# Performance work log

Hardware: AMD Instinct MI355X
Metric: run time of the kernel (lower is better)

The kernel has to match this reference:

```python
import jax, jax.numpy as jnp
import numpy as np

BN_EPS = 1e-5


def setup_inputs() -> dict:
    key = jax.random.key(0)
    ks = jax.random.split(key, 12)
    B, C, S, M = 128, 512, 128, 512  # batch, model_dim, spatial_size, middle_ss
    lim_in = 1.0 / np.sqrt(S)   # torch Linear init bound, fan_in = S
    lim_mid = 1.0 / np.sqrt(M)
    return {
        "query": jax.random.normal(ks[0], (B, C, S), jnp.float32),
        "key":   jax.random.normal(ks[1], (B, C, S), jnp.float32),
        "value": jax.random.normal(ks[2], (B, C, S), jnp.float32),
        "Wq": jax.random.uniform(ks[3], (M, S), jnp.float32, -lim_in, lim_in),
        "bq": jax.random.uniform(ks[4], (M,), jnp.float32, -lim_in, lim_in),
        "Wk": jax.random.uniform(ks[5], (M, S), jnp.float32, -lim_in, lim_in),
        "bk": jax.random.uniform(ks[6], (M,), jnp.float32, -lim_in, lim_in),
        "Wv": jax.random.uniform(ks[7], (M, S), jnp.float32, -lim_in, lim_in),
        "bv": jax.random.uniform(ks[8], (M,), jnp.float32, -lim_in, lim_in),
        "Wf": jax.random.uniform(ks[9], (S, M), jnp.float32, -lim_mid, lim_mid),
        "bf": jax.random.uniform(ks[10], (S,), jnp.float32, -lim_mid, lim_mid),
        "gamma": jnp.ones((C,), jnp.float32),
        "beta": jnp.zeros((C,), jnp.float32),
    }


def reference(query, key, value, Wq, bq, Wk, bk, Wv, bv, Wf, bf, gamma, beta):
    residual = value                                  # [B, C, S]
    q = jnp.einsum('bcs,ms->bcm', query, Wq) + bq     # [B, C, M]
    k = jnp.einsum('bcs,ms->bcm', key, Wk) + bk
    v = jnp.einsum('bcs,ms->bcm', value, Wv) + bv
    scale = k.shape[-1] ** (-0.5)
    scores = jnp.einsum('bim,bjm->bij', q, k) * scale  # [B, C, C]
    attention = jax.nn.softmax(scores, axis=2)
    context = jnp.einsum('bij,bjm->bim', attention, v)  # [B, C, M]
    out = jnp.einsum('bcm,sm->bcs', context, Wf) + bf    # [B, C, S]
    # BatchNorm1d (training mode): stats over (batch, spatial) per channel
    mean = jnp.mean(out, axis=(0, 2), keepdims=True)
    var = jnp.mean(jnp.square(out - mean), axis=(0, 2), keepdims=True)
    out = (out - mean) * jax.lax.rsqrt(var + BN_EPS)
    out = out * gamma[None, :, None] + beta[None, :, None]
    out = jax.nn.relu(out)
    out = residual + out
    return (out, attention)
```

## Files before the change

### kernel.cpp

```cpp
#include <hip/hip_runtime.h>
#include <math.h>

#define B_  128
#define C_  512
#define S_  128
#define M_  512
#define BN_EPS 1e-5f

typedef __attribute__((ext_vector_type(8))) short   short8;
typedef __attribute__((ext_vector_type(4))) float   floatx4;
typedef __attribute__((ext_vector_type(4))) unsigned short ushort4v;

__device__ __forceinline__ unsigned short f2bu(float f) {
    union { float f; unsigned int u; } c; c.f = f;
    unsigned int u = c.u;
    return (unsigned short)((u + 0x7fffu + ((u >> 16) & 1u)) >> 16);
}

__global__ __launch_bounds__(256)
void f2bf_kernel(const float* __restrict__ in, unsigned short* __restrict__ out, long n8)
{
    const long i = (long)blockIdx.x * 256 + threadIdx.x;
    if (i >= n8) return;
    const float4* p = (const float4*)in + 2 * i;
    const float4 x = p[0], y = p[1];
    ushort4v u0, u1;
    u0.x = f2bu(x.x); u0.y = f2bu(x.y); u0.z = f2bu(x.z); u0.w = f2bu(x.w);
    u1.x = f2bu(y.x); u1.y = f2bu(y.y); u1.z = f2bu(y.z); u1.w = f2bu(y.w);
    ((ushort4v*)out)[2 * i]     = u0;
    ((ushort4v*)out)[2 * i + 1] = u1;
}

__global__ __launch_bounds__(256)
void gemm_bf16(const unsigned short* __restrict__ A, const unsigned short* __restrict__ Bm,
               const float* __restrict__ bias, void* __restrict__ Cc,
               int M, int N, int K, int ldA, int ldB, int ldC,
               long sA, long sB, long sC, float scale, int outMode)
{
    const int bz = blockIdx.z;
    A  += (long)bz * sA;
    Bm += (long)bz * sB;

    __shared__ unsigned short As[128][72];
    __shared__ unsigned short Bs[128][72];

    const int t    = threadIdx.x;
    const int lane = t & 63;
    const int wave = t >> 6;
    const int wm   = (wave >> 1) * 64;
    const int wn   = (wave & 1) * 64;
    const int lrow = lane & 15;
    const int quad = lane >> 4;
    const int row0 = blockIdx.x * 128;
    const int col0 = blockIdx.y * 128;

    floatx4 acc[4][4] = {};

    const int srow = t >> 3;
    const int skc  = (t & 7) * 8;

    for (int k0 = 0; k0 < K; k0 += 64) {
        #pragma unroll
        for (int i = 0; i < 4; ++i) {
            const int r = srow + i * 32;
            *(short8*)&As[r][skc] =
                *(const short8*)(A + (long)(row0 + r) * ldA + k0 + skc);
            *(short8*)&Bs[r][skc] =
                *(const short8*)(Bm + (long)(col0 + r) * ldB + k0 + skc);
        }
        __syncthreads();

        #pragma unroll
        for (int kb = 0; kb < 2; ++kb) {
            short8 af[4], bfr[4];
            #pragma unroll
            for (int i = 0; i < 4; ++i)
                af[i]  = *(const short8*)&As[wm + i * 16 + lrow][kb * 32 + quad * 8];
            #pragma unroll
            for (int j = 0; j < 4; ++j)
                bfr[j] = *(const short8*)&Bs[wn + j * 16 + lrow][kb * 32 + quad * 8];
            #pragma unroll
            for (int i = 0; i < 4; ++i)
                #pragma unroll
                for (int j = 0; j < 4; ++j)
                    acc[i][j] = __builtin_amdgcn_mfma_f32_16x16x32_bf16(
                        af[i], bfr[j], acc[i][j], 0, 0, 0);
        }
        __syncthreads();
    }

    #pragma unroll
    for (int j = 0; j < 4; ++j) {
        const int col = col0 + wn + j * 16 + lrow;
        const float bv = bias ? bias[col] : 0.0f;
        #pragma unroll
        for (int i = 0; i < 4; ++i) {
            const int rbase = row0 + wm + i * 16 + quad * 4;
            #pragma unroll
            for (int reg = 0; reg < 4; ++reg) {
                const float val = acc[i][j][reg] * scale + bv;
                const int r = rbase + reg;
                if (outMode == 0) {
                    ((float*)Cc)[(long)bz * sC + (long)r * ldC + col] = val;
                } else if (outMode == 1) {
                    ((unsigned short*)Cc)[(long)bz * sC + (long)r * ldC + col] = f2bu(val);
                } else {
                    ((unsigned short*)Cc)[((long)(r >> 9)) * 65536 + (long)col * 512 + (r & 511)] = f2bu(val);
                }
            }
        }
    }
}

__global__ __launch_bounds__(256)
void softmax_kernel(float* __restrict__ attn, unsigned short* __restrict__ attn_bf)
{
    const int row  = blockIdx.x * 4 + (threadIdx.x >> 6);
    const int lane = threadIdx.x & 63;
    float4* p = (float4*)(attn + (long)row * 512);

    float4 a = p[lane];
    float4 b = p[lane + 64];

    float mx = fmaxf(fmaxf(fmaxf(a.x, a.y), fmaxf(a.z, a.w)),
                     fmaxf(fmaxf(b.x, b.y), fmaxf(b.z, b.w)));
    #pragma unroll
    for (int off = 1; off < 64; off <<= 1)
        mx = fmaxf(mx, __shfl_xor(mx, off));

    a.x = expf(a.x - mx); a.y = expf(a.y - mx);
    a.z = expf(a.z - mx); a.w = expf(a.w - mx);
    b.x = expf(b.x - mx); b.y = expf(b.y - mx);
    b.z = expf(b.z - mx); b.w = expf(b.w - mx);

    float sum = a.x + a.y + a.z + a.w + b.x + b.y + b.z + b.w;
    #pragma unroll
    for (int off = 1; off < 64; off <<= 1)
        sum += __shfl_xor(sum, off);

    const float inv = 1.0f / sum;
    a.x *= inv; a.y *= inv; a.z *= inv; a.w *= inv;
    b.x *= inv; b.y *= inv; b.z *= inv; b.w *= inv;

    p[lane]      = a;
    p[lane + 64] = b;

    ushort4v u0, u1;
    u0.x = f2bu(a.x); u0.y = f2bu(a.y); u0.z = f2bu(a.z); u0.w = f2bu(a.w);
    u1.x = f2bu(b.x); u1.y = f2bu(b.y); u1.z = f2bu(b.z); u1.w = f2bu(b.w);
    ushort4v* q = (ushort4v*)(attn_bf + (long)row * 512);
    q[lane]      = u0;
    q[lane + 64] = u1;
}

__global__ __launch_bounds__(256)
void bn_stats_kernel(const float* __restrict__ outp, float* __restrict__ stats)
{
    const int c   = blockIdx.x;
    const int tid = threadIdx.x;
    float s = 0.f, ss = 0.f;
    for (int idx = tid; idx < B_ * S_; idx += 256) {
        const int b  = idx >> 7;
        const int sp = idx & 127;
        const float x = outp[((long)b * C_ + c) * S_ + sp];
        s  += x;
        ss += x * x;
    }
    __shared__ float shs[256];
    __shared__ float shss[256];
    shs[tid] = s; shss[tid] = ss;
    __syncthreads();
    for (int off = 128; off > 0; off >>= 1) {
        if (tid < off) { shs[tid] += shs[tid + off]; shss[tid] += shss[tid + off]; }
        __syncthreads();
    }
    if (tid == 0) {
        const float n    = (float)(B_ * S_);
        const float mean = shs[0] / n;
        const float var  = shss[0] / n - mean * mean;
        stats[c]      = mean;
        stats[C_ + c] = rsqrtf(var + BN_EPS);
    }
}

__global__ __launch_bounds__(256)
void bn_apply_kernel(const float* __restrict__ outp, const float* __restrict__ value,
                     const float* __restrict__ stats, const float* __restrict__ gamma,
                     const float* __restrict__ beta, float* __restrict__ out)
{
    const long i4 = (long)blockIdx.x * 256 + threadIdx.x;
    const int  c  = (int)((i4 >> 5) & (C_ - 1));

    const float mean = stats[c];
    const float istd = stats[C_ + c];
    const float g    = gamma[c] * istd;
    const float bc   = beta[c] - mean * g;

    const float4 x = ((const float4*)outp)[i4];
    const float4 r = ((const float4*)value)[i4];
    float4 y;
    y.x = fmaxf(fmaf(x.x, g, bc), 0.f) + r.x;
    y.y = fmaxf(fmaf(x.y, g, bc), 0.f) + r.y;
    y.z = fmaxf(fmaf(x.z, g, bc), 0.f) + r.z;
    y.w = fmaxf(fmaf(x.w, g, bc), 0.f) + r.w;
    ((float4*)out)[i4] = y;
}

extern "C" void kernel_launch(void* const* d_in, const int* in_sizes, int n_in,
                              void* d_out, int out_size, void* d_ws, size_t ws_size,
                              hipStream_t stream)
{
    const float* query = (const float*)d_in[0];
    const float* key   = (const float*)d_in[1];
    const float* value = (const float*)d_in[2];
    const float* Wq    = (const float*)d_in[3];
    const float* bq    = (const float*)d_in[4];
    const float* Wk    = (const float*)d_in[5];
    const float* bk    = (const float*)d_in[6];
    const float* Wv    = (const float*)d_in[7];
    const float* bv    = (const float*)d_in[8];
    const float* Wf    = (const float*)d_in[9];
    const float* bf    = (const float*)d_in[10];
    const float* gamma = (const float*)d_in[11];
    const float* beta  = (const float*)d_in[12];

    const long BC  = (long)B_ * C_;
    const long BCM = BC * M_;
    const long BCS = BC * S_;
    const long BCC = BC * C_;

    unsigned short* w      = (unsigned short*)d_ws;
    unsigned short* q_bf   = w;
    unsigned short* k_bf   = q_bf + BCM;
    unsigned short* v2_bf  = k_bf + BCM;
    unsigned short* attnbf = v2_bf + BCM;
    unsigned short* vwT    = attnbf + BCC;
    unsigned short* qin    = vwT + (long)B_ * S_ * C_;
    unsigned short* kin    = qin + BCS;
    unsigned short* vin    = kin + BCS;
    unsigned short* Wq_bf  = vin + BCS;
    unsigned short* Wk_bf  = Wq_bf + (long)M_ * S_;
    unsigned short* Wv_bf  = Wk_bf + (long)M_ * S_;
    unsigned short* Wf_bf  = Wv_bf + (long)M_ * S_;
    float* outp  = (float*)(Wf_bf + (long)S_ * M_);
    float* stats = outp + BCS;

    float* out0 = (float*)d_out;
    float* attn = out0 + BCS;

    const float scale = 1.0f / sqrtf((float)M_);
    dim3 blk(256);

    f2bf_kernel<<<dim3(BCS / 8 / 256), blk, 0, stream>>>(query, qin, BCS / 8);
    f2bf_kernel<<<dim3(BCS / 8 / 256), blk, 0, stream>>>(key,   kin, BCS / 8);
    f2bf_kernel<<<dim3(BCS / 8 / 256), blk, 0, stream>>>(value, vin, BCS / 8);
    f2bf_kernel<<<dim3(32), blk, 0, stream>>>(Wq, Wq_bf, (long)M_ * S_ / 8);
    f2bf_kernel<<<dim3(32), blk, 0, stream>>>(Wk, Wk_bf, (long)M_ * S_ / 8);
    f2bf_kernel<<<dim3(32), blk, 0, stream>>>(Wv, Wv_bf, (long)M_ * S_ / 8);
    f2bf_kernel<<<dim3(32), blk, 0, stream>>>(Wf, Wf_bf, (long)S_ * M_ / 8);

    gemm_bf16<<<dim3(512, 4, 1), blk, 0, stream>>>(
        qin, Wq_bf, bq, q_bf,  (int)BC, M_, S_, S_, S_, M_, 0, 0, 0, 1.0f, 1);
    gemm_bf16<<<dim3(512, 4, 1), blk, 0, stream>>>(
        kin, Wk_bf, bk, k_bf,  (int)BC, M_, S_, S_, S_, M_, 0, 0, 0, 1.0f, 1);
    gemm_bf16<<<dim3(512, 4, 1), blk, 0, stream>>>(
        vin, Wv_bf, bv, v2_bf, (int)BC, M_, S_, S_, S_, M_, 0, 0, 0, 1.0f, 1);

    gemm_bf16<<<dim3(4, 4, 128), blk, 0, stream>>>(
        q_bf, k_bf, nullptr, attn, C_, C_, M_, M_, M_, C_,
        (long)C_ * M_, (long)C_ * M_, (long)C_ * C_, scale, 0);

    softmax_kernel<<<dim3(BC / 4), blk, 0, stream>>>(attn, attnbf);

    gemm_bf16<<<dim3(512, 1, 1), blk, 0, stream>>>(
        v2_bf, Wf_bf, bf, vwT, (int)BC, S_, M_, M_, M_, 0, 0, 0, 0, 1.0f, 2);

    gemm_bf16<<<dim3(4, 1, 128), blk, 0, stream>>>(
        attnbf, vwT, nullptr, outp, C_, S_, C_, C_, C_, S_,
        (long)C_ * C_, (long)S_ * C_, (long)C_ * S_, 1.0f, 0);

    bn_stats_kernel<<<dim3(C_), blk, 0, stream>>>(outp, stats);

    bn_apply_kernel<<<dim3(BCS / 4 / 256), blk, 0, stream>>>(
        outp, value, stats, gamma, beta, out0);
}
```

Baseline: 649.0 us.

## Fuse scores GEMM with softmax, use direct-to-LDS loads with swizzle, batch conversions

Replaces the separate scores GEMM and softmax kernels with one 1024-thread kernel. It computes a 128x512 score tile per block and does the row max and sum through shared-memory reductions, so the fp32 scores are no longer written and then read back. The generic GEMM now loads straight into LDS via global_load_lds with an XOR-swizzled layout instead of padding, and carries occupancy hints. The Wf projection is recast so vwT comes out in a plain row-major layout without the scattered transposed stores. The seven fp32-to-bf16 conversion launches are merged into two, trading fewer launches for more complex kernels and higher register/LDS pressure.

```diff
diff --git a/kernel.cpp b/kernel.cpp
--- a/kernel.cpp
+++ b/kernel.cpp
@@ -17,11 +17,25 @@
     return (unsigned short)((u + 0x7fffu + ((u >> 16) & 1u)) >> 16);
 }
 
+__device__ __forceinline__ void gload_lds16(const unsigned short* g, unsigned short* l)
+{
+    __builtin_amdgcn_global_load_lds(
+        (const __attribute__((address_space(1))) unsigned int*)g,
+        (__attribute__((address_space(3))) unsigned int*)l,
+        16, 0, 0);
+}
+
 __global__ __launch_bounds__(256)
-void f2bf_kernel(const float* __restrict__ in, unsigned short* __restrict__ out, long n8)
+void f2bf3_kernel(const float* __restrict__ q, const float* __restrict__ k,
+                  const float* __restrict__ v,
+                  unsigned short* __restrict__ qo, unsigned short* __restrict__ ko,
+                  unsigned short* __restrict__ vo)
 {
     const long i = (long)blockIdx.x * 256 + threadIdx.x;
-    if (i >= n8) return;
+    const float* in; unsigned short* out;
+    if (blockIdx.y == 0)      { in = q; out = qo; }
+    else if (blockIdx.y == 1) { in = k; out = ko; }
+    else                      { in = v; out = vo; }
     const float4* p = (const float4*)in + 2 * i;
     const float4 x = p[0], y = p[1];
     ushort4v u0, u1;
@@ -32,17 +46,40 @@
 }
 
 __global__ __launch_bounds__(256)
-void gemm_bf16(const unsigned short* __restrict__ A, const unsigned short* __restrict__ Bm,
+void f2bfw_kernel(const float* __restrict__ w0, const float* __restrict__ w1,
+                  const float* __restrict__ w2, const float* __restrict__ w3,
+                  unsigned short* __restrict__ o0, unsigned short* __restrict__ o1,
+                  unsigned short* __restrict__ o2, unsigned short* __restrict__ o3)
+{
+    const long i = (long)blockIdx.x * 256 + threadIdx.x;
+    const float* in; unsigned short* out;
+    if (blockIdx.y == 0)      { in = w0; out = o0; }
+    else if (blockIdx.y == 1) { in = w1; out = o1; }
+    else if (blockIdx.y == 2) { in = w2; out = o2; }
+    else                      { in = w3; out = o3; }
+    const float4* p = (const float4*)in + 2 * i;
+    const float4 x = p[0], y = p[1];
+    ushort4v u0, u1;
+    u0.x = f2bu(x.x); u0.y = f2bu(x.y); u0.z = f2bu(x.z); u0.w = f2bu(x.w);
+    u1.x = f2bu(y.x); u1.y = f2bu(y.y); u1.z = f2bu(y.z); u1.w = f2bu(y.w);
+    ((ushort4v*)out)[2 * i]     = u0;
+    ((ushort4v*)out)[2 * i + 1] = u1;
+}
+
+__global__ __launch_bounds__(256, 4)
+void gemm_bf16(const unsigned short* __restrict__ A,
+               const unsigned short* __restrict__ Bm,
                const float* __restrict__ bias, void* __restrict__ Cc,
-               int M, int N, int K, int ldA, int ldB, int ldC,
-               long sA, long sB, long sC, float scale, int outMode)
+               int K, int ldA, int ldB, int ldC,
+               long sA, long sB, long sC, float scale,
+               int outMode, int biasRow)
 {
     const int bz = blockIdx.z;
     A  += (long)bz * sA;
     Bm += (long)bz * sB;
 
-    __shared__ unsigned short As[128][72];
-    __shared__ unsigned short Bs[128][72];
+    __shared__ __attribute__((aligned(16))) unsigned short As[128 * 64];
+    __shared__ __attribute__((aligned(16))) unsigned short Bs[128 * 64];
 
     const int t    = threadIdx.x;
     const int lane = t & 63;
@@ -54,37 +91,41 @@
     const int row0 = blockIdx.x * 128;
     const int col0 = blockIdx.y * 128;
 
+    const int slr = lane >> 3;
+    const int scg = (lane & 7) ^ slr;
+
     floatx4 acc[4][4] = {};
 
-    const int srow = t >> 3;
-    const int skc  = (t & 7) * 8;
-
     for (int k0 = 0; k0 < K; k0 += 64) {
         #pragma unroll
         for (int i = 0; i < 4; ++i) {
-            const int r = srow + i * 32;
-            *(short8*)&As[r][skc] =
-                *(const short8*)(A + (long)(row0 + r) * ldA + k0 + skc);
-            *(short8*)&Bs[r][skc] =
-                *(const short8*)(Bm + (long)(col0 + r) * ldB + k0 + skc);
+            const int r = wave * 32 + i * 8 + slr;
+            gload_lds16(A  + (long)(row0 + r) * ldA + k0 + scg * 8,
+                        As + (wave * 256 + i * 64) * 8);
+            gload_lds16(Bm + (long)(col0 + r) * ldB + k0 + scg * 8,
+                        Bs + (wave * 256 + i * 64) * 8);
         }
         __syncthreads();
 
         #pragma unroll
         for (int kb = 0; kb < 2; ++kb) {
-            short8 af[4], bfr[4];
-            #pragma unroll
-            for (int i = 0; i < 4; ++i)
-                af[i]  = *(const short8*)&As[wm + i * 16 + lrow][kb * 32 + quad * 8];
-            #pragma unroll
-            for (int j = 0; j < 4; ++j)
-                bfr[j] = *(const short8*)&Bs[wn + j * 16 + lrow][kb * 32 + quad * 8];
-            #pragma unroll
-            for (int i = 0; i < 4; ++i)
+            short8 af[4];
+            #pragma unroll
+            for (int i = 0; i < 4; ++i) {
+                const int r  = wm + i * 16 + lrow;
+                const int pg = r * 8 + ((kb * 4 + quad) ^ (r & 7));
+                af[i] = *(const short8*)(As + pg * 8);
+            }
+            #pragma unroll
+            for (int j = 0; j < 4; ++j) {
+                const int r  = wn + j * 16 + lrow;
+                const int pg = r * 8 + ((kb * 4 + quad) ^ (r & 7));
+                const short8 bf8 = *(const short8*)(Bs + pg * 8);
                 #pragma unroll
-                for (int j = 0; j < 4; ++j)
+                for (int i = 0; i < 4; ++i)
                     acc[i][j] = __builtin_amdgcn_mfma_f32_16x16x32_bf16(
-                        af[i], bfr[j], acc[i][j], 0, 0, 0);
+                        af[i], bf8, acc[i][j], 0, 0, 0);
+            }
         }
         __syncthreads();
     }
@@ -92,65 +133,153 @@
     #pragma unroll
     for (int j = 0; j < 4; ++j) {
         const int col = col0 + wn + j * 16 + lrow;
-        const float bv = bias ? bias[col] : 0.0f;
         #pragma unroll
         for (int i = 0; i < 4; ++i) {
             const int rbase = row0 + wm + i * 16 + quad * 4;
             #pragma unroll
             for (int reg = 0; reg < 4; ++reg) {
-                const float val = acc[i][j][reg] * scale + bv;
                 const int r = rbase + reg;
-                if (outMode == 0) {
-                    ((float*)Cc)[(long)bz * sC + (long)r * ldC + col] = val;
-                } else if (outMode == 1) {
-                    ((unsigned short*)Cc)[(long)bz * sC + (long)r * ldC + col] = f2bu(val);
-                } else {
-                    ((unsigned short*)Cc)[((long)(r >> 9)) * 65536 + (long)col * 512 + (r & 511)] = f2bu(val);
-                }
+                float v = acc[i][j][reg] * scale;
+                if (bias) v += biasRow ? bias[r] : bias[col];
+                if (outMode == 0)
+                    ((float*)Cc)[(long)bz * sC + (long)r * ldC + col] = v;
+                else
+                    ((unsigned short*)Cc)[(long)bz * sC + (long)r * ldC + col] = f2bu(v);
             }
         }
     }
 }
 
-__global__ __launch_bounds__(256)
-void softmax_kernel(float* __restrict__ attn, unsigned short* __restrict__ attn_bf)
-{
-    const int row  = blockIdx.x * 4 + (threadIdx.x >> 6);
-    const int lane = threadIdx.x & 63;
-    float4* p = (float4*)(attn + (long)row * 512);
-
-    float4 a = p[lane];
-    float4 b = p[lane + 64];
-
-    float mx = fmaxf(fmaxf(fmaxf(a.x, a.y), fmaxf(a.z, a.w)),
-                     fmaxf(fmaxf(b.x, b.y), fmaxf(b.z, b.w)));
+__global__ __launch_bounds__(1024, 4)
+void scores_softmax(const unsigned short* __restrict__ Q,
+                    const unsigned short* __restrict__ Kb,
+                    float* __restrict__ attn, unsigned short* __restrict__ attnbf,
+                    float scale)
+{
+    const int b    = blockIdx.y;
+    const int row0 = blockIdx.x * 128;
+    Q      += ((long)b * C_ + row0) * M_;
+    Kb     += (long)b * C_ * M_;
+    attn   += (long)b * C_ * C_;
+    attnbf += (long)b * C_ * C_;
+
+    __shared__ __attribute__((aligned(16))) unsigned short Qs[128 * 32];
+    __shared__ __attribute__((aligned(16))) unsigned short Ks[512 * 32];
+    __shared__ float red[128][8];
+
+    const int t    = threadIdx.x;
+    const int lane = t & 63;
+    const int wave = t >> 6;
+    const int wr   = wave >> 3;
+    const int wc   = wave & 7;
+    const int lrow = lane & 15;
+    const int quad = lane >> 4;
+
+    const int slr = lane >> 2;
+    const int scg = (lane & 3) ^ (slr & 3);
+
+    floatx4 acc[4][4] = {};
+
+    for (int k0 = 0; k0 < M_; k0 += 32) {
+        #pragma unroll
+        for (int ii = 0; ii < 2; ++ii) {
+            const int idx = wave * 2 + ii;
+            const int r   = idx * 16 + slr;
+            gload_lds16(Kb + (long)r * M_ + k0 + scg * 8,
+                        Ks + idx * 512);
+        }
+        if (wave < 8) {
+            const int r = wave * 16 + slr;
+            gload_lds16(Q + (long)r * M_ + k0 + scg * 8,
+                        Qs + wave * 512);
+        }
+        __syncthreads();
+
+        short8 af[4];
+        #pragma unroll
+        for (int i = 0; i < 4; ++i) {
+            const int r  = wr * 64 + i * 16 + lrow;
+            const int pg = r * 4 + (quad ^ (r & 3));
+            af[i] = *(const short8*)(Qs + pg * 8);
+        }
+        #pragma unroll
+        for (int j = 0; j < 4; ++j) {
+            const int r  = wc * 64 + j * 16 + lrow;
+            const int pg = r * 4 + (quad ^ (r & 3));
+            const short8 bf8 = *(const short8*)(Ks + pg * 8);
+            #pragma unroll
+            for (int i = 0; i < 4; ++i)
+                acc[i][j] = __builtin_amdgcn_mfma_f32_16x16x32_bf16(
+                    af[i], bf8, acc[i][j], 0, 0, 0);
+        }
+        __syncthreads();
+    }
+
     #pragma unroll
-    for (int off = 1; off < 64; off <<= 1)
-        mx = fmaxf(mx, __shfl_xor(mx, off));
-
-    a.x = expf(a.x - mx); a.y = expf(a.y - mx);
-    a.z = expf(a.z - mx); a.w = expf(a.w - mx);
-    b.x = expf(b.x - mx); b.y = expf(b.y - mx);
-    b.z = expf(b.z - mx); b.w = expf(b.w - mx);
-
-    float sum = a.x + a.y + a.z + a.w + b.x + b.y + b.z + b.w;
+    for (int i = 0; i < 4; ++i)
+        #pragma unroll
+        for (int reg = 0; reg < 4; ++reg) {
+            float m = fmaxf(fmaxf(acc[i][0][reg], acc[i][1][reg]),
+                            fmaxf(acc[i][2][reg], acc[i][3][reg]));
+            #pragma unroll
+            for (int off = 1; off < 16; off <<= 1)
+                m = fmaxf(m, __shfl_xor(m, off));
+            if (lrow == 0)
+                red[wr * 64 + i * 16 + quad * 4 + reg][wc] = m;
+        }
+    __syncthreads();
+
+    float mrow[4][4];
     #pragma unroll
-    for (int off = 1; off < 64; off <<= 1)
-        sum += __shfl_xor(sum, off);
-
-    const float inv = 1.0f / sum;
-    a.x *= inv; a.y *= inv; a.z *= inv; a.w *= inv;
-    b.x *= inv; b.y *= inv; b.z *= inv; b.w *= inv;
-
-    p[lane]      = a;
-    p[lane + 64] = b;
-
-    ushort4v u0, u1;
-    u0.x = f2bu(a.x); u0.y = f2bu(a.y); u0.z = f2bu(a.z); u0.w = f2bu(a.w);
-    u1.x = f2bu(b.x); u1.y = f2bu(b.y); u1.z = f2bu(b.z); u1.w = f2bu(b.w);
-    ushort4v* q = (ushort4v*)(attn_bf + (long)row * 512);
-    q[lane]      = u0;
-    q[lane + 64] = u1;
+    for (int i = 0; i < 4; ++i)
+        #pragma unroll
+        for (int reg = 0; reg < 4; ++reg) {
+            const int r = wr * 64 + i * 16 + quad * 4 + reg;
+            const float4 a = *(const float4*)&red[r][0];
+            const float4 b = *(const float4*)&red[r][4];
+            mrow[i][reg] = fmaxf(fmaxf(fmaxf(a.x, a.y), fmaxf(a.z, a.w)),
+                                 fmaxf(fmaxf(b.x, b.y), fmaxf(b.z, b.w)));
+        }
+    __syncthreads();
+
+    const float c2 = scale * 1.44269504088896f;
+    #pragma unroll
+    for (int i = 0; i < 4; ++i)
+        #pragma unroll
+        for (int reg = 0; reg < 4; ++reg) {
+            float s = 0.f;
+            #pragma unroll
+            for (int j = 0; j < 4; ++j) {
+                const float e = exp2f((acc[i][j][reg] - mrow[i][reg]) * c2);
+                acc[i][j][reg] = e;
+                s += e;
+            }
+            #pragma unroll
+            for (int off = 1; off < 16; off <<= 1)
+                s += __shfl_xor(s, off);
+            if (lrow == 0)
+                red[wr * 64 + i * 16 + quad * 4 + reg][wc] = s;
+        }
+    __syncthreads();
+
+    #pragma unroll
+    for (int i = 0; i < 4; ++i)
+        #pragma unroll
+        for (int reg = 0; reg < 4; ++reg) {
+            const int rl = wr * 64 + i * 16 + quad * 4 + reg;
+            const float4 a = *(const float4*)&red[rl][0];
+            const float4 b = *(const float4*)&red[rl][4];
+            const float sum = (a.x + a.y + a.z + a.w) + (b.x + b.y + b.z + b.w);
+            const float inv = 1.0f / sum;
+            const long rowoff = (long)(row0 + rl) * C_;
+            #pragma unroll
+            for (int j = 0; j < 4; ++j) {
+                const int col = wc * 64 + j * 16 + lrow;
+                const float v = acc[i][j][reg] * inv;
+                attn[rowoff + col]   = v;
+                attnbf[rowoff + col] = f2bu(v);
+            }
+        }
 }
 
 __global__ __launch_bounds__(256)
@@ -235,7 +364,7 @@
     unsigned short* v2_bf  = k_bf + BCM;
     unsigned short* attnbf = v2_bf + BCM;
     unsigned short* vwT    = attnbf + BCC;
-    unsigned short* qin    = vwT + (long)B_ * S_ * C_;
+    unsigned short* qin    = vwT + BCS;
     unsigned short* kin    = qin + BCS;
     unsigned short* vin    = kin + BCS;
     unsigned short* Wq_bf  = vin + BCS;
@@ -251,33 +380,27 @@
     const float scale = 1.0f / sqrtf((float)M_);
     dim3 blk(256);
 
-    f2bf_kernel<<<dim3(BCS / 8 / 256), blk, 0, stream>>>(query, qin, BCS / 8);
-    f2bf_kernel<<<dim3(BCS / 8 / 256), blk, 0, stream>>>(key,   kin, BCS / 8);
-    f2bf_kernel<<<dim3(BCS / 8 / 256), blk, 0, stream>>>(value, vin, BCS / 8);
-    f2bf_kernel<<<dim3(32), blk, 0, stream>>>(Wq, Wq_bf, (long)M_ * S_ / 8);
-    f2bf_kernel<<<dim3(32), blk, 0, stream>>>(Wk, Wk_bf, (long)M_ * S_ / 8);
-    f2bf_kernel<<<dim3(32), blk, 0, stream>>>(Wv, Wv_bf, (long)M_ * S_ / 8);
-    f2bf_kernel<<<dim3(32), blk, 0, stream>>>(Wf, Wf_bf, (long)S_ * M_ / 8);
+    f2bf3_kernel<<<dim3(BCS / 8 / 256, 3), blk, 0, stream>>>(
+        query, key, value, qin, kin, vin);
+    f2bfw_kernel<<<dim3(32, 4), blk, 0, stream>>>(
+        Wq, Wk, Wv, Wf, Wq_bf, Wk_bf, Wv_bf, Wf_bf);
 
     gemm_bf16<<<dim3(512, 4, 1), blk, 0, stream>>>(
-        qin, Wq_bf, bq, q_bf,  (int)BC, M_, S_, S_, S_, M_, 0, 0, 0, 1.0f, 1);
+        qin, Wq_bf, bq, q_bf,  S_, S_, S_, M_, 0, 0, 0, 1.0f, 1, 0);
     gemm_bf16<<<dim3(512, 4, 1), blk, 0, stream>>>(
-        kin, Wk_bf, bk, k_bf,  (int)BC, M_, S_, S_, S_, M_, 0, 0, 0, 1.0f, 1);
+        kin, Wk_bf, bk, k_bf,  S_, S_, S_, M_, 0, 0, 0, 1.0f, 1, 0);
     gemm_bf16<<<dim3(512, 4, 1), blk, 0, stream>>>(
-        vin, Wv_bf, bv, v2_bf, (int)BC, M_, S_, S_, S_, M_, 0, 0, 0, 1.0f, 1);
-
-    gemm_bf16<<<dim3(4, 4, 128), blk, 0, stream>>>(
-        q_bf, k_bf, nullptr, attn, C_, C_, M_, M_, M_, C_,
-        (long)C_ * M_, (long)C_ * M_, (long)C_ * C_, scale, 0);
-
-    softmax_kernel<<<dim3(BC / 4), blk, 0, stream>>>(attn, attnbf);
-
-    gemm_bf16<<<dim3(512, 1, 1), blk, 0, stream>>>(
-        v2_bf, Wf_bf, bf, vwT, (int)BC, S_, M_, M_, M_, 0, 0, 0, 0, 1.0f, 2);
-
-    gemm_bf16<<<dim3(4, 1, 128), blk, 0, stream>>>(
-        attnbf, vwT, nullptr, outp, C_, S_, C_, C_, C_, S_,
-        (long)C_ * C_, (long)S_ * C_, (long)C_ * S_, 1.0f, 0);
+        vin, Wv_bf, bv, v2_bf, S_, S_, S_, M_, 0, 0, 0, 1.0f, 1, 0);
+
+    scores_softmax<<<dim3(C_ / 128, B_), dim3(1024), 0, stream>>>(
+        q_bf, k_bf, attn, attnbf, scale);
+
+    gemm_bf16<<<dim3(1, 512, 1), blk, 0, stream>>>(
+        Wf_bf, v2_bf, bf, vwT, M_, M_, M_, (int)BC, 0, 0, 0, 1.0f, 1, 1);
+
+    gemm_bf16<<<dim3(C_ / 128, 1, B_), blk, 0, stream>>>(
+        attnbf, vwT, nullptr, outp, C_, C_, (int)BC, S_,
+        (long)C_ * C_, (long)C_, (long)C_ * S_, 1.0f, 0, 0);
 
     bn_stats_kernel<<<dim3(C_), blk, 0, stream>>>(outp, stats);
 
```

New measurement: 698.9 us. 7.7% more time.
